# Optimization experiments

Measured on AMD Instinct MI355X. Metric: run time of the kernel, lower is better.

Reference implementation:

```python
import jax, jax.numpy as jnp
import numpy as np

N_NODES = 50000
N_EDGES = 800000
D_IN = 128
D_OUT = 128
LN_EPS = 1e-5


def setup_inputs() -> dict:
    key = jax.random.key(0)
    ks = jax.random.split(key, 8)
    h = jax.random.normal(ks[0], (N_NODES, D_IN), dtype=jnp.float32)
    edge_row = jax.random.randint(ks[1], (N_EDGES,), 0, N_NODES, dtype=jnp.int32)
    edge_col = jax.random.randint(ks[2], (N_EDGES,), 0, N_NODES, dtype=jnp.int32)
    # normalized-ish edge weights (e.g. 1/deg values in GraphSAGE-mean)
    edge_val = jax.random.uniform(ks[3], (N_EDGES,), dtype=jnp.float32) / 16.0
    scale = 1.0 / np.sqrt(D_IN)
    W_self = jax.random.normal(ks[4], (D_OUT, D_IN), dtype=jnp.float32) * scale
    b_self = jnp.zeros((D_OUT,), dtype=jnp.float32)
    W_neigh = jax.random.normal(ks[5], (D_OUT, D_IN), dtype=jnp.float32) * scale
    b_neigh = jnp.zeros((D_OUT,), dtype=jnp.float32)
    ln_gamma = jnp.ones((2 * D_OUT,), dtype=jnp.float32)
    ln_beta = jnp.zeros((2 * D_OUT,), dtype=jnp.float32)
    return {"h": h, "edge_row": edge_row, "edge_col": edge_col, "edge_val": edge_val,
            "W_self": W_self, "b_self": b_self, "W_neigh": W_neigh, "b_neigh": b_neigh,
            "ln_gamma": ln_gamma, "ln_beta": ln_beta}


def reference(h, edge_row, edge_col, edge_val, W_self, b_self, W_neigh, b_neigh, ln_gamma, ln_beta):
    out_nodes = N_NODES  # adj.sizes()[0]
    # support = adj.spmm(h): gather source features, scale by edge value, scatter-add to dest rows
    msgs = h[edge_col] * edge_val[:, None]                      # [E, D_IN]
    support = jax.ops.segment_sum(msgs, edge_row, num_segments=out_nodes)  # [N, D_IN]
    self_h = h[:out_nodes] @ W_self.T + b_self                  # [N, D_OUT]
    neigh_h = support @ W_neigh.T + b_neigh                     # [N, D_OUT]
    x = jnp.concatenate([self_h, neigh_h], axis=1)              # [N, 2*D_OUT]
    x = jax.nn.relu(x)
    # LayerNorm over last dim, elementwise affine
    mu = jnp.mean(x, axis=-1, keepdims=True)
    var = jnp.mean(jnp.square(x - mu), axis=-1, keepdims=True)
    x = (x - mu) * jax.lax.rsqrt(var + LN_EPS)
    return x * ln_gamma + ln_beta
```

## Files before the change

### kernel.cpp

```cpp
#include <hip/hip_runtime.h>
#include <hip/hip_fp16.h>
#include <cstddef>

#define DIN 128
#define BKROWS 64
#define EPB 4096
#define MAXB 1024
#define RCAP 32
#define LCAP 1536
#define NRUNMAX 256

typedef short bf16x8 __attribute__((ext_vector_type(8)));
typedef float f32x4  __attribute__((ext_vector_type(4)));

__device__ inline unsigned short f2bf(float x) {
    union { float f; unsigned u; } v; v.f = x;
    unsigned r = v.u + 0x7FFFu + ((v.u >> 16) & 1u);
    return (unsigned short)(r >> 16);
}
__device__ inline float bf_lo(unsigned x) { return __int_as_float(x << 16); }
__device__ inline float bf_hi(unsigned x) { return __int_as_float(x & 0xFFFF0000u); }


__global__ __launch_bounds__(256) void prep_bin(
    const float* __restrict__ h, const int* __restrict__ erow,
    const int* __restrict__ ecol, const float* __restrict__ evalv,
    const float* __restrict__ Ws, const float* __restrict__ Wn,
    unsigned short* __restrict__ hb, unsigned short* __restrict__ wbf,
    int2* __restrict__ recs, int* __restrict__ cnt2,
    int n_conv, int n_edges, int nbkt, int nbb, int pb)
{
    __shared__ int cur[MAXB];
    const int t = threadIdx.x;
    const int bid = blockIdx.x;

    if (bid < nbb) {
        for (int i = t; i < nbkt; i += 256) cur[i] = 0;
        __syncthreads();
        int s = bid * EPB;
        int e = s + EPB; if (e > n_edges) e = n_edges;
        for (int i = s + t; i < e; i += 256) {
            int r = erow[i];
            int bk = r >> 6;
            int off = atomicAdd(&cur[bk], 1);
            if (off < RCAP) {
                unsigned short vb = __half_as_ushort(__float2half_rn(evalv[i]));
                int2 rec;
                rec.x = r & (BKROWS - 1);
                rec.y = (int)((unsigned)(ecol[i] & 0xFFFF) | ((unsigned)vb << 16));
                recs[((size_t)bk * nbb + bid) * RCAP + off] = rec;
            }
        }
        __syncthreads();
        for (int i = t; i < nbkt; i += 256) {
            int hc = cur[i]; if (hc > RCAP) hc = RCAP;
            cnt2[(size_t)i * nbb + bid] = hc;
        }
        return;
    }

    int cb = bid - nbb;
    if (cb < pb) {
        int i = cb * 256 + t;
        if (i < n_conv) {
            const float4* p = (const float4*)(h + (size_t)i * 8);
            float4 a = p[0], bq = p[1];
            bf16x8 v;
            v[0] = f2bf(a.x);  v[1] = f2bf(a.y);  v[2] = f2bf(a.z);  v[3] = f2bf(a.w);
            v[4] = f2bf(bq.x); v[5] = f2bf(bq.y); v[6] = f2bf(bq.z); v[7] = f2bf(bq.w);
            *(bf16x8*)(hb + (size_t)i * 8) = v;
        }
    } else {
        int wi = (cb - pb) * 256 + t;
        if (wi < 4096) {
            const float* src = (wi < 2048) ? (Ws + (size_t)wi * 8)
                                           : (Wn + (size_t)(wi - 2048) * 8);
            const float4* p = (const float4*)src;
            float4 a = p[0], bq = p[1];
            bf16x8 v;
            v[0] = f2bf(a.x);  v[1] = f2bf(a.y);  v[2] = f2bf(a.z);  v[3] = f2bf(a.w);
            v[4] = f2bf(bq.x); v[5] = f2bf(bq.y); v[6] = f2bf(bq.z); v[7] = f2bf(bq.w);
            *(bf16x8*)(wbf + (size_t)wi * 8) = v;
        }
    }
}

__global__ __launch_bounds__(512) void row_gather(
    const int2* __restrict__ recs, const int* __restrict__ cnt2,
    const unsigned short* __restrict__ hb, unsigned short* __restrict__ support,
    int n_nodes, int nbb)
{
    __shared__ int2 lrec[LCAP];
    __shared__ unsigned plist[LCAP];
    __shared__ int rcn[NRUNMAX];
    __shared__ int rbase[NRUNMAX];
    __shared__ int ebase[NRUNMAX];
    __shared__ int cnt[BKROWS], lbase[BKROWS], cur[BKROWS];

    const int t = threadIdx.x;
    const int b = blockIdx.x;
    const int wave = t >> 6;
    const int lane = t & 63;

    int rc = 0;
    if (t < NRUNMAX) {
        if (t < nbb) {
            rc = cnt2[(size_t)b * nbb + t];
            if (rc > RCAP) rc = RCAP;
        }
        rcn[t] = rc;
        rbase[t] = rc;
    }
    __syncthreads();
    for (int off = 1; off < NRUNMAX; off <<= 1) {
        int v = (t < NRUNMAX && t >= off) ? rbase[t - off] : 0;
        __syncthreads();
        if (t < NRUNMAX) rbase[t] += v;
        __syncthreads();
    }
    if (t < NRUNMAX) ebase[t] = rbase[t] - rcn[t];
    if (t < BKROWS) { cnt[t] = 0; cur[t] = 0; }
    __syncthreads();
    int tot = rbase[NRUNMAX - 1];
    if (tot > LCAP) tot = LCAP;

    for (int j = (t >> 3); j < nbb; j += 64) {
        int c = rcn[j];
        int dst = ebase[j];
        const int2* rp = recs + ((size_t)b * nbb + j) * RCAP;
        for (int i = (t & 7); i < c; i += 8)
            if (dst + i < LCAP) lrec[dst + i] = rp[i];
    }
    __syncthreads();

    for (int i = t; i < tot; i += 512)
        atomicAdd(&cnt[lrec[i].x], 1);
    __syncthreads();

    if (t < BKROWS) lbase[t] = cnt[t];
    __syncthreads();
    for (int off = 1; off < BKROWS; off <<= 1) {
        int v = (t < BKROWS && t >= off) ? lbase[t - off] : 0;
        __syncthreads();
        if (t < BKROWS) lbase[t] += v;
        __syncthreads();
    }
    if (t < BKROWS) lbase[t] -= cnt[t];
    __syncthreads();

    for (int i = t; i < tot; i += 512) {
        int2 rec = lrec[i];
        int pos = lbase[rec.x] + atomicAdd(&cur[rec.x], 1);
        plist[pos] = (unsigned)rec.y;
    }
    __syncthreads();

    const unsigned* hu = (const unsigned*)hb;

#pragma unroll
    for (int rr = 0; rr < 8; rr++) {
        int r = wave * 8 + rr;
        int s = lbase[r];
        int e2 = s + cnt[r];

        float ax[8], ay[8];
#pragma unroll
        for (int k = 0; k < 8; k++) { ax[k] = 0.f; ay[k] = 0.f; }

        int e = s;
        for (; e + 7 < e2; e += 8) {
            unsigned p[8];
#pragma unroll
            for (int k = 0; k < 8; k++) p[k] = plist[e + k];
            unsigned x[8];
#pragma unroll
            for (int k = 0; k < 8; k++)
                x[k] = hu[(size_t)(p[k] & 0xFFFFu) * 64 + lane];
#pragma unroll
            for (int k = 0; k < 8; k++) {
                float v = __half2float(__ushort_as_half((unsigned short)(p[k] >> 16)));
                ax[k] += bf_lo(x[k]) * v;
                ay[k] += bf_hi(x[k]) * v;
            }
        }
        for (; e + 3 < e2; e += 4) {
            unsigned p[4];
#pragma unroll
            for (int k = 0; k < 4; k++) p[k] = plist[e + k];
            unsigned x[4];
#pragma unroll
            for (int k = 0; k < 4; k++)
                x[k] = hu[(size_t)(p[k] & 0xFFFFu) * 64 + lane];
#pragma unroll
            for (int k = 0; k < 4; k++) {
                float v = __half2float(__ushort_as_half((unsigned short)(p[k] >> 16)));
                ax[k] += bf_lo(x[k]) * v;
                ay[k] += bf_hi(x[k]) * v;
            }
        }
        for (; e < e2; e++) {
            unsigned p = plist[e];
            unsigned x = hu[(size_t)(p & 0xFFFFu) * 64 + lane];
            float v = __half2float(__ushort_as_half((unsigned short)(p >> 16)));
            ax[0] += bf_lo(x) * v; ay[0] += bf_hi(x) * v;
        }

        float sx = 0.f, sy = 0.f;
#pragma unroll
        for (int k = 0; k < 8; k++) { sx += ax[k]; sy += ay[k]; }

        int row = b * BKROWS + r;
        if (row < n_nodes) {
            unsigned outp = (unsigned)f2bf(sx) | ((unsigned)f2bf(sy) << 16);
            ((unsigned*)support)[(size_t)row * 64 + lane] = outp;
        }
    }
}

__global__ __launch_bounds__(256) void mfma_gemm_ln(
    const unsigned short* __restrict__ hb,
    const unsigned short* __restrict__ support,
    const unsigned short* __restrict__ wbf,
    const float* __restrict__ bs, const float* __restrict__ bn,
    const float* __restrict__ gamma, const float* __restrict__ beta,
    float* __restrict__ out,
    int n_nodes)
{
    __shared__ short Wlds[2][128][128];

    const int tid = threadIdx.x;

    {
        const uint4* wsrc = (const uint4*)wbf;
#pragma unroll
        for (int j = 0; j < 16; j++) {
            int i = j * 256 + tid;
            int m = i >> 11;
            int d = (i >> 4) & 127;
            int ch = i & 15;
            int phys = ch ^ (d & 7);
            *(uint4*)&Wlds[m][d][phys * 8] = wsrc[i];
        }
    }
    __syncthreads();

    const int wave = tid >> 6;
    const int lane = tid & 63;
    const int q = lane >> 4;
    const int c = lane & 15;
    const int n0 = blockIdx.x * 64 + wave * 16;
    if (n0 >= n_nodes) return;

    f32x4 accS[8], accN[8];
#pragma unroll
    for (int t = 0; t < 8; t++) {
        accS[t] = (f32x4){0.f, 0.f, 0.f, 0.f};
        accN[t] = (f32x4){0.f, 0.f, 0.f, 0.f};
    }

    const bf16x8* ph = (const bf16x8*)(hb + (size_t)(n0 + c) * DIN + q * 8);
    const bf16x8* ps = (const bf16x8*)(support + (size_t)(n0 + c) * DIN + q * 8);

#pragma unroll
    for (int ks = 0; ks < 4; ks++) {
        bf16x8 aH = ph[ks * 4];
        bf16x8 aS = ps[ks * 4];
        int cl = ks * 4 + q;
#pragma unroll
        for (int t = 0; t < 8; t++) {
            int d = t * 16 + c;
            int phys = cl ^ (d & 7);
            bf16x8 bS = *(const bf16x8*)&Wlds[0][d][phys * 8];
            accS[t] = __builtin_amdgcn_mfma_f32_16x16x32_bf16(aH, bS, accS[t], 0, 0, 0);
            bf16x8 bN = *(const bf16x8*)&Wlds[1][d][phys * 8];
            accN[t] = __builtin_amdgcn_mfma_f32_16x16x32_bf16(aS, bN, accN[t], 0, 0, 0);
        }
    }

    float sum[4] = {0.f, 0.f, 0.f, 0.f};
    float ssq[4] = {0.f, 0.f, 0.f, 0.f};
#pragma unroll
    for (int t = 0; t < 8; t++) {
        float bS = bs[t * 16 + c];
        float bN = bn[t * 16 + c];
#pragma unroll
        for (int r = 0; r < 4; r++) {
            float v1 = accS[t][r] + bS; v1 = v1 > 0.f ? v1 : 0.f; accS[t][r] = v1;
            float v2 = accN[t][r] + bN; v2 = v2 > 0.f ? v2 : 0.f; accN[t][r] = v2;
            sum[r] += v1 + v2;
            ssq[r] += v1 * v1 + v2 * v2;
        }
    }
#pragma unroll
    for (int off = 8; off >= 1; off >>= 1) {
#pragma unroll
        for (int r = 0; r < 4; r++) {
            sum[r] += __shfl_xor(sum[r], off, 64);
            ssq[r] += __shfl_xor(ssq[r], off, 64);
        }
    }
    float mu[4], rstd[4];
#pragma unroll
    for (int r = 0; r < 4; r++) {
        mu[r] = sum[r] * (1.f / 256.f);
        float var = ssq[r] * (1.f / 256.f) - mu[r] * mu[r];
        rstd[r] = rsqrtf(var + 1e-5f);
    }

#pragma unroll
    for (int t = 0; t < 8; t++) {
        int dS = t * 16 + c;
        int dN = 128 + t * 16 + c;
        float gS = gamma[dS], btS = beta[dS];
        float gN = gamma[dN], btN = beta[dN];
#pragma unroll
        for (int r = 0; r < 4; r++) {
            size_t rowbase = (size_t)(n0 + q * 4 + r) * 256;
            out[rowbase + dS] = (accS[t][r] - mu[r]) * rstd[r] * gS + btS;
            out[rowbase + dN] = (accN[t][r] - mu[r]) * rstd[r] * gN + btN;
        }
    }
}

extern "C" void kernel_launch(void* const* d_in, const int* in_sizes, int n_in,
                              void* d_out, int out_size, void* d_ws, size_t ws_size,
                              hipStream_t stream)
{
    const float* h     = (const float*)d_in[0];
    const int*   erow  = (const int*)d_in[1];
    const int*   ecol  = (const int*)d_in[2];
    const float* evalv = (const float*)d_in[3];
    const float* Ws    = (const float*)d_in[4];
    const float* bs    = (const float*)d_in[5];
    const float* Wn    = (const float*)d_in[6];
    const float* bn    = (const float*)d_in[7];
    const float* gamma = (const float*)d_in[8];
    const float* beta  = (const float*)d_in[9];
    float* out = (float*)d_out;

    int n_nodes = in_sizes[0] / DIN;
    int n_edges = in_sizes[1];

    int nbkt = (n_nodes + BKROWS - 1) / BKROWS;
    int nbb  = (n_edges + EPB - 1) / EPB;

    char* ws = (char*)d_ws;
    unsigned short* hb      = (unsigned short*)ws;  ws += (size_t)n_nodes * DIN * sizeof(short);
    unsigned short* support = (unsigned short*)ws;  ws += (size_t)n_nodes * DIN * sizeof(short);
    unsigned short* wbf = (unsigned short*)ws;      ws += (size_t)2 * 128 * 128 * sizeof(short);
    int2* recs = (int2*)ws;                         ws += (size_t)nbkt * nbb * RCAP * sizeof(int2);
    int* cnt2  = (int*)ws;                          ws += (size_t)nbkt * nbb * sizeof(int);

    int n_conv = n_nodes * DIN / 8;
    int pb = (n_conv + 255) / 256;

    prep_bin  <<<nbb + pb + 16, 256, 0, stream>>>(h, erow, ecol, evalv, Ws, Wn,
                                                  hb, wbf, recs, cnt2,
                                                  n_conv, n_edges, nbkt, nbb, pb);
    row_gather<<<nbkt, 512, 0, stream>>>(recs, cnt2, hb, support, n_nodes, nbb);

    int gb = (n_nodes + 63) / 64;
    mfma_gemm_ln<<<gb, 256, 0, stream>>>(hb, support, wbf, bs, bn, gamma, beta,
                                         out, n_nodes);
}
```

Baseline: 170.9 us.

## Fuse row gather with MFMA GEMM and LayerNorm, pre-pack weights in fragment order

Merges the gather kernel and the GEMM+LayerNorm kernel into one. The aggregated support tile now stays in LDS and is never written to or re-read from global memory. Weights are pre-packed in prep_bin into MFMA B-fragment order so each lane reads them directly from global or L2, with no LDS weight staging. The 8 waves split the self and neighbour halves, and LayerNorm statistics are combined through LDS. The cost is a heavier fused kernel with more LDS and register pressure, and weights are re-read from cache by every block.

```diff
diff --git a/kernel.cpp b/kernel.cpp
--- a/kernel.cpp
+++ b/kernel.cpp
@@ -26,7 +26,7 @@
     const float* __restrict__ h, const int* __restrict__ erow,
     const int* __restrict__ ecol, const float* __restrict__ evalv,
     const float* __restrict__ Ws, const float* __restrict__ Wn,
-    unsigned short* __restrict__ hb, unsigned short* __restrict__ wbf,
+    unsigned short* __restrict__ hb, unsigned short* __restrict__ wpk,
     int2* __restrict__ recs, int* __restrict__ cnt2,
     int n_conv, int n_edges, int nbkt, int nbb, int pb)
 {
@@ -73,29 +73,42 @@
     } else {
         int wi = (cb - pb) * 256 + t;
         if (wi < 4096) {
-            const float* src = (wi < 2048) ? (Ws + (size_t)wi * 8)
-                                           : (Wn + (size_t)(wi - 2048) * 8);
+            int m    = wi >> 11;
+            int ks   = (wi >> 9) & 3;
+            int tt   = (wi >> 6) & 7;
+            int lane = wi & 63;
+            int q    = lane >> 4;
+            int c    = lane & 15;
+            int d    = tt * 16 + c;
+            int col0 = (ks * 4 + q) * 8;
+            const float* src = (m == 0 ? Ws : Wn) + (size_t)d * 128 + col0;
             const float4* p = (const float4*)src;
             float4 a = p[0], bq = p[1];
             bf16x8 v;
             v[0] = f2bf(a.x);  v[1] = f2bf(a.y);  v[2] = f2bf(a.z);  v[3] = f2bf(a.w);
             v[4] = f2bf(bq.x); v[5] = f2bf(bq.y); v[6] = f2bf(bq.z); v[7] = f2bf(bq.w);
-            *(bf16x8*)(wbf + (size_t)wi * 8) = v;
+            *(bf16x8*)(wpk + (size_t)wi * 8) = v;
         }
     }
 }
 
-__global__ __launch_bounds__(512) void row_gather(
+__global__ __launch_bounds__(512, 6) void gather_gemm_ln(
     const int2* __restrict__ recs, const int* __restrict__ cnt2,
-    const unsigned short* __restrict__ hb, unsigned short* __restrict__ support,
+    const unsigned short* __restrict__ hb, const unsigned short* __restrict__ wpk,
+    const float* __restrict__ bs, const float* __restrict__ bn,
+    const float* __restrict__ gamma, const float* __restrict__ beta,
+    float* __restrict__ out,
     int n_nodes, int nbb)
 {
     __shared__ int2 lrec[LCAP];
     __shared__ unsigned plist[LCAP];
+    __shared__ short sup[BKROWS][DIN];
     __shared__ int rcn[NRUNMAX];
     __shared__ int rbase[NRUNMAX];
     __shared__ int ebase[NRUNMAX];
-    __shared__ int cnt[BKROWS], lbase[BKROWS], cur[BKROWS];
+    __shared__ int cnt[BKROWS], lbase[BKROWS], curw[BKROWS];
+    __shared__ float lsum[2][BKROWS];
+    __shared__ float lssq[2][BKROWS];
 
     const int t = threadIdx.x;
     const int b = blockIdx.x;
@@ -119,7 +132,7 @@
         __syncthreads();
     }
     if (t < NRUNMAX) ebase[t] = rbase[t] - rcn[t];
-    if (t < BKROWS) { cnt[t] = 0; cur[t] = 0; }
+    if (t < BKROWS) { cnt[t] = 0; curw[t] = 0; }
     __syncthreads();
     int tot = rbase[NRUNMAX - 1];
     if (tot > LCAP) tot = LCAP;
@@ -150,12 +163,13 @@
 
     for (int i = t; i < tot; i += 512) {
         int2 rec = lrec[i];
-        int pos = lbase[rec.x] + atomicAdd(&cur[rec.x], 1);
+        int pos = lbase[rec.x] + atomicAdd(&curw[rec.x], 1);
         plist[pos] = (unsigned)rec.y;
     }
     __syncthreads();
 
     const unsigned* hu = (const unsigned*)hb;
+    unsigned* sup32 = (unsigned*)sup;
 
 #pragma unroll
     for (int rr = 0; rr < 8; rr++) {
@@ -209,115 +223,90 @@
 #pragma unroll
         for (int k = 0; k < 8; k++) { sx += ax[k]; sy += ay[k]; }
 
-        int row = b * BKROWS + r;
-        if (row < n_nodes) {
-            unsigned outp = (unsigned)f2bf(sx) | ((unsigned)f2bf(sy) << 16);
-            ((unsigned*)support)[(size_t)row * 64 + lane] = outp;
-        }
-    }
-}
-
-__global__ __launch_bounds__(256) void mfma_gemm_ln(
-    const unsigned short* __restrict__ hb,
-    const unsigned short* __restrict__ support,
-    const unsigned short* __restrict__ wbf,
-    const float* __restrict__ bs, const float* __restrict__ bn,
-    const float* __restrict__ gamma, const float* __restrict__ beta,
-    float* __restrict__ out,
-    int n_nodes)
-{
-    __shared__ short Wlds[2][128][128];
-
-    const int tid = threadIdx.x;
-
-    {
-        const uint4* wsrc = (const uint4*)wbf;
-#pragma unroll
-        for (int j = 0; j < 16; j++) {
-            int i = j * 256 + tid;
-            int m = i >> 11;
-            int d = (i >> 4) & 127;
-            int ch = i & 15;
-            int phys = ch ^ (d & 7);
-            *(uint4*)&Wlds[m][d][phys * 8] = wsrc[i];
-        }
-    }
-    __syncthreads();
-
-    const int wave = tid >> 6;
-    const int lane = tid & 63;
+        sup32[r * 64 + lane] = (unsigned)f2bf(sx) | ((unsigned)f2bf(sy) << 16);
+    }
+    __syncthreads();
+
+    const int side = wave >> 2;
+    const int g = wave & 3;
     const int q = lane >> 4;
     const int c = lane & 15;
-    const int n0 = blockIdx.x * 64 + wave * 16;
-    if (n0 >= n_nodes) return;
-
-    f32x4 accS[8], accN[8];
-#pragma unroll
-    for (int t = 0; t < 8; t++) {
-        accS[t] = (f32x4){0.f, 0.f, 0.f, 0.f};
-        accN[t] = (f32x4){0.f, 0.f, 0.f, 0.f};
-    }
-
-    const bf16x8* ph = (const bf16x8*)(hb + (size_t)(n0 + c) * DIN + q * 8);
-    const bf16x8* ps = (const bf16x8*)(support + (size_t)(n0 + c) * DIN + q * 8);
-
-#pragma unroll
-    for (int ks = 0; ks < 4; ks++) {
-        bf16x8 aH = ph[ks * 4];
-        bf16x8 aS = ps[ks * 4];
-        int cl = ks * 4 + q;
-#pragma unroll
-        for (int t = 0; t < 8; t++) {
-            int d = t * 16 + c;
-            int phys = cl ^ (d & 7);
-            bf16x8 bS = *(const bf16x8*)&Wlds[0][d][phys * 8];
-            accS[t] = __builtin_amdgcn_mfma_f32_16x16x32_bf16(aH, bS, accS[t], 0, 0, 0);
-            bf16x8 bN = *(const bf16x8*)&Wlds[1][d][phys * 8];
-            accN[t] = __builtin_amdgcn_mfma_f32_16x16x32_bf16(aS, bN, accN[t], 0, 0, 0);
-        }
-    }
-
-    float sum[4] = {0.f, 0.f, 0.f, 0.f};
-    float ssq[4] = {0.f, 0.f, 0.f, 0.f};
-#pragma unroll
-    for (int t = 0; t < 8; t++) {
-        float bS = bs[t * 16 + c];
-        float bN = bn[t * 16 + c];
+    const int n0 = b * 64 + g * 16;
+    const bool active = (n0 < n_nodes);
+
+    f32x4 acc[8];
+#pragma unroll
+    for (int tt = 0; tt < 8; tt++) acc[tt] = (f32x4){0.f, 0.f, 0.f, 0.f};
+
+    if (active) {
+        const bf16x8* pa = (side == 0)
+            ? (const bf16x8*)(hb + (size_t)(n0 + c) * DIN + q * 8)
+            : (const bf16x8*)(&sup[g * 16 + c][q * 8]);
+        const bf16x8* pb = (const bf16x8*)wpk + (size_t)side * 2048 + lane;
+
+#pragma unroll
+        for (int ks = 0; ks < 4; ks++) {
+            bf16x8 aA = pa[ks * 4];
+#pragma unroll
+            for (int tt = 0; tt < 8; tt++) {
+                bf16x8 bB = pb[(ks * 8 + tt) * 64];
+                acc[tt] = __builtin_amdgcn_mfma_f32_16x16x32_bf16(aA, bB, acc[tt], 0, 0, 0);
+            }
+        }
+
+        float sum[4] = {0.f, 0.f, 0.f, 0.f};
+        float ssq[4] = {0.f, 0.f, 0.f, 0.f};
+        const float* bias = (side == 0) ? bs : bn;
+#pragma unroll
+        for (int tt = 0; tt < 8; tt++) {
+            float bv = bias[tt * 16 + c];
+#pragma unroll
+            for (int r = 0; r < 4; r++) {
+                float v1 = acc[tt][r] + bv; v1 = v1 > 0.f ? v1 : 0.f; acc[tt][r] = v1;
+                sum[r] += v1;
+                ssq[r] += v1 * v1;
+            }
+        }
+#pragma unroll
+        for (int off = 8; off >= 1; off >>= 1) {
+#pragma unroll
+            for (int r = 0; r < 4; r++) {
+                sum[r] += __shfl_xor(sum[r], off, 64);
+                ssq[r] += __shfl_xor(ssq[r], off, 64);
+            }
+        }
+        if (c == 0) {
+#pragma unroll
+            for (int r = 0; r < 4; r++) {
+                lsum[side][g * 16 + q * 4 + r] = sum[r];
+                lssq[side][g * 16 + q * 4 + r] = ssq[r];
+            }
+        }
+    }
+    __syncthreads();
+
+    if (active) {
+        float mu[4], rstd[4];
 #pragma unroll
         for (int r = 0; r < 4; r++) {
-            float v1 = accS[t][r] + bS; v1 = v1 > 0.f ? v1 : 0.f; accS[t][r] = v1;
-            float v2 = accN[t][r] + bN; v2 = v2 > 0.f ? v2 : 0.f; accN[t][r] = v2;
-            sum[r] += v1 + v2;
-            ssq[r] += v1 * v1 + v2 * v2;
-        }
-    }
-#pragma unroll
-    for (int off = 8; off >= 1; off >>= 1) {
-#pragma unroll
-        for (int r = 0; r < 4; r++) {
-            sum[r] += __shfl_xor(sum[r], off, 64);
-            ssq[r] += __shfl_xor(ssq[r], off, 64);
-        }
-    }
-    float mu[4], rstd[4];
-#pragma unroll
-    for (int r = 0; r < 4; r++) {
-        mu[r] = sum[r] * (1.f / 256.f);
-        float var = ssq[r] * (1.f / 256.f) - mu[r] * mu[r];
-        rstd[r] = rsqrtf(var + 1e-5f);
-    }
-
-#pragma unroll
-    for (int t = 0; t < 8; t++) {
-        int dS = t * 16 + c;
-        int dN = 128 + t * 16 + c;
-        float gS = gamma[dS], btS = beta[dS];
-        float gN = gamma[dN], btN = beta[dN];
-#pragma unroll
-        for (int r = 0; r < 4; r++) {
-            size_t rowbase = (size_t)(n0 + q * 4 + r) * 256;
-            out[rowbase + dS] = (accS[t][r] - mu[r]) * rstd[r] * gS + btS;
-            out[rowbase + dN] = (accN[t][r] - mu[r]) * rstd[r] * gN + btN;
+            int idx = g * 16 + q * 4 + r;
+            float s2 = lsum[0][idx] + lsum[1][idx];
+            float q2 = lssq[0][idx] + lssq[1][idx];
+            mu[r] = s2 * (1.f / 256.f);
+            float var = q2 * (1.f / 256.f) - mu[r] * mu[r];
+            rstd[r] = rsqrtf(var + 1e-5f);
+        }
+
+        const int dofs = side * 128;
+#pragma unroll
+        for (int tt = 0; tt < 8; tt++) {
+            int d = dofs + tt * 16 + c;
+            float gv = gamma[d], btv = beta[d];
+#pragma unroll
+            for (int r = 0; r < 4; r++) {
+                size_t rowbase = (size_t)(n0 + q * 4 + r) * 256;
+                out[rowbase + d] = (acc[tt][r] - mu[r]) * rstd[r] * gv + btv;
+            }
         }
     }
 }
@@ -345,21 +334,17 @@
     int nbb  = (n_edges + EPB - 1) / EPB;
 
     char* ws = (char*)d_ws;
-    unsigned short* hb      = (unsigned short*)ws;  ws += (size_t)n_nodes * DIN * sizeof(short);
-    unsigned short* support = (unsigned short*)ws;  ws += (size_t)n_nodes * DIN * sizeof(short);
-    unsigned short* wbf = (unsigned short*)ws;      ws += (size_t)2 * 128 * 128 * sizeof(short);
-    int2* recs = (int2*)ws;                         ws += (size_t)nbkt * nbb * RCAP * sizeof(int2);
-    int* cnt2  = (int*)ws;                          ws += (size_t)nbkt * nbb * sizeof(int);
+    unsigned short* hb  = (unsigned short*)ws;  ws += (size_t)n_nodes * DIN * sizeof(short);
+    unsigned short* wpk = (unsigned short*)ws;  ws += (size_t)2 * 128 * 128 * sizeof(short);
+    int2* recs = (int2*)ws;                     ws += (size_t)nbkt * nbb * RCAP * sizeof(int2);
+    int* cnt2  = (int*)ws;                      ws += (size_t)nbkt * nbb * sizeof(int);
 
     int n_conv = n_nodes * DIN / 8;
     int pb = (n_conv + 255) / 256;
 
-    prep_bin  <<<nbb + pb + 16, 256, 0, stream>>>(h, erow, ecol, evalv, Ws, Wn,
-                                                  hb, wbf, recs, cnt2,
-                                                  n_conv, n_edges, nbkt, nbb, pb);
-    row_gather<<<nbkt, 512, 0, stream>>>(recs, cnt2, hb, support, n_nodes, nbb);
-
-    int gb = (n_nodes + 63) / 64;
-    mfma_gemm_ln<<<gb, 256, 0, stream>>>(hb, support, wbf, bs, bn, gamma, beta,
-                                         out, n_nodes);
+    prep_bin      <<<nbb + pb + 16, 256, 0, stream>>>(h, erow, ecol, evalv, Ws, Wn,
+                                                      hb, wpk, recs, cnt2,
+                                                      n_conv, n_edges, nbkt, nbb, pb);
+    gather_gemm_ln<<<nbkt, 512, 0, stream>>>(recs, cnt2, hb, wpk, bs, bn,
+                                             gamma, beta, out, n_nodes, nbb);
 }
```

Result: slower. 186.0 us (+8.8%).
